# Kernel optimization log

Measured on AMD Instinct MI355X. Metric: run time of the kernel, lower is better.

Reference implementation:

```python
import jax, jax.numpy as jnp
import numpy as np

N, E, B = 50000, 400000, 64
N_INC, E_OUTC, U_INC, G_INC = 64, 64, 32, 64
H1A, H1B = 128, 64           # node_model_mlp1_hidden_sizes
H2 = 256                     # node_model_mlp2_hidden_sizes[0]
DIM_LH, DIM_L, N_OUTC = 128, 32, 64
LN_EPS = 1e-5

def _lin_init(key, din, dout):
    k1, k2 = jax.random.split(key)
    bound = 1.0 / np.sqrt(din)
    W = jax.random.uniform(k1, (din, dout), jnp.float32, -bound, bound)
    b = jax.random.uniform(k2, (dout,), jnp.float32, -bound, bound)
    return W, b

def setup_inputs() -> dict:
    key = jax.random.key(0)
    ks = jax.random.split(key, 16)
    x = jax.random.normal(ks[0], (N, N_INC), jnp.float32)
    edge_index = jax.random.randint(ks[1], (2, E), 0, N, jnp.int64)
    edge_attr = jax.random.normal(ks[2], (E, E_OUTC), jnp.float32)
    u = jax.random.normal(ks[3], (B, U_INC), jnp.float32)
    batch = jnp.sort(jax.random.randint(ks[4], (N,), 0, B, jnp.int64))
    goal = jax.random.normal(ks[5], (N, G_INC), jnp.float32)
    W1, b1 = _lin_init(ks[6], N_INC + E_OUTC, H1A)
    g1, be1 = jnp.ones((H1A,), jnp.float32), jnp.zeros((H1A,), jnp.float32)
    W2, b2 = _lin_init(ks[7], H1A, H1B)
    mlp2_inc = N_INC + H1B + U_INC
    W3, b3 = _lin_init(ks[8], mlp2_inc, H2)
    g3, be3 = jnp.ones((H2,), jnp.float32), jnp.zeros((H2,), jnp.float32)
    W4, b4 = _lin_init(ks[9], H2, DIM_LH)
    g4, be4 = jnp.ones((DIM_LH,), jnp.float32), jnp.zeros((DIM_LH,), jnp.float32)
    Wm, bm = _lin_init(ks[10], DIM_LH, DIM_L)
    Wv, bv = _lin_init(ks[11], DIM_LH, DIM_L)
    Wx, bx = _lin_init(ks[12], DIM_L, N_OUTC)
    return dict(x=x, edge_index=edge_index, edge_attr=edge_attr, u=u, batch=batch,
                goal=goal, W1=W1, b1=b1, g1=g1, be1=be1, W2=W2, b2=b2,
                W3=W3, b3=b3, g3=g3, be3=be3, W4=W4, b4=b4, g4=g4, be4=be4,
                Wm=Wm, bm=bm, Wv=Wv, bv=bv, Wx=Wx, bx=bx)

def _layernorm(h, g, b):
    mu = jnp.mean(h, axis=-1, keepdims=True)
    var = jnp.var(h, axis=-1, keepdims=True)
    return (h - mu) * jax.lax.rsqrt(var + LN_EPS) * g + b

def reference(x, edge_index, edge_attr, u, batch, goal,
              W1, b1, g1, be1, W2, b2,
              W3, b3, g3, be3, W4, b4, g4, be4,
              Wm, bm, Wv, bv, Wx, bx):
    row, col = edge_index[0], edge_index[1]
    # --- edge MLP: gather x[row], concat edge_attr, 2-layer MLP with LN+ReLU
    se = jnp.concatenate([x[row], edge_attr], axis=1)          # [E, n_inc+e_outc]
    h = jax.nn.relu(_layernorm(se @ W1 + b1, g1, be1)) @ W2 + b2  # [E, H1B]
    # --- scatter_mean over destination nodes
    sums = jax.ops.segment_sum(h, col, num_segments=N)          # [N, H1B]
    cnts = jax.ops.segment_sum(jnp.ones((E,), h.dtype), col, num_segments=N)
    aggs = sums / jnp.maximum(cnts, 1.0)[:, None]
    # --- node MLP 2
    z = jnp.concatenate([x, aggs, u[batch]], axis=1)            # [N, mlp2_inc]
    z = jax.nn.relu(_layernorm(z @ W3 + b3, g3, be3))
    z = jax.nn.relu(_layernorm(z @ W4 + b4, g4, be4))           # [N, DIM_LH]
    z_mu = z @ Wm + bm
    z_var = z @ Wv + bv                                         # log-variance
    eps = jax.random.normal(jax.random.key(42), z_mu.shape, z_mu.dtype)
    z_s = z_mu + eps * jnp.exp(0.5 * z_var)                     # reparameterize
    out = z_s @ Wx + bx                                         # [N, n_outc]
    return (out, z_mu, z_var)
```

## Files before the change

### kernel.cpp

```cpp
#include <hip/hip_runtime.h>

#define NN 50000
#define EE 400000
#define NB 49

typedef __attribute__((ext_vector_type(8))) short bf16x8;
typedef __attribute__((ext_vector_type(4))) float f32x4;

__device__ __forceinline__ void fma4(float4& a, float s, const float4& w){
  a.x = fmaf(s, w.x, a.x);
  a.y = fmaf(s, w.y, a.y);
  a.z = fmaf(s, w.z, a.z);
  a.w = fmaf(s, w.w, a.w);
}

__device__ __forceinline__ unsigned short f2bf(float f){
  unsigned u = __float_as_uint(f);
  unsigned r = (u + 0x7fffu + ((u >> 16) & 1u)) >> 16;
  return (unsigned short)r;
}

__device__ __forceinline__ bf16x8 cvt8(float4 lo, float4 hi){
  bf16x8 r;
  r[0]=(short)f2bf(lo.x); r[1]=(short)f2bf(lo.y); r[2]=(short)f2bf(lo.z); r[3]=(short)f2bf(lo.w);
  r[4]=(short)f2bf(hi.x); r[5]=(short)f2bf(hi.y); r[6]=(short)f2bf(hi.z); r[7]=(short)f2bf(hi.w);
  return r;
}

__device__ __forceinline__ unsigned packhl(float v){
  unsigned hi = f2bf(v);
  float fh = __uint_as_float(hi << 16);
  unsigned lo = f2bf(v - fh);
  return (hi << 16) | lo;
}

__device__ __forceinline__ uint4 pack4(float4 v){
  uint4 p;
  p.x = packhl(v.x); p.y = packhl(v.y); p.z = packhl(v.z); p.w = packhl(v.w);
  return p;
}

__device__ __forceinline__ void unpack8(uint4 p0, uint4 p1, bf16x8& hi, bf16x8& lo){
  hi[0]=(short)(p0.x>>16); lo[0]=(short)(p0.x & 0xffffu);
  hi[1]=(short)(p0.y>>16); lo[1]=(short)(p0.y & 0xffffu);
  hi[2]=(short)(p0.z>>16); lo[2]=(short)(p0.z & 0xffffu);
  hi[3]=(short)(p0.w>>16); lo[3]=(short)(p0.w & 0xffffu);
  hi[4]=(short)(p1.x>>16); lo[4]=(short)(p1.x & 0xffffu);
  hi[5]=(short)(p1.y>>16); lo[5]=(short)(p1.y & 0xffffu);
  hi[6]=(short)(p1.z>>16); lo[6]=(short)(p1.z & 0xffffu);
  hi[7]=(short)(p1.w>>16); lo[7]=(short)(p1.w & 0xffffu);
}

__device__ __forceinline__ unsigned rotl32(unsigned v, int d){ return (v<<d)|(v>>(32-d)); }

__device__ __forceinline__ float eps_at(unsigned idx){
  const unsigned k0 = 0u, k1 = 42u, k2 = 0x1BD11BDAu ^ 0u ^ 42u;
  unsigned x0 = 0u + k0, x1 = idx + k1;
  const int rotA[4] = {13,15,26,6};
  const int rotB[4] = {17,29,16,24};
  #pragma unroll
  for (int i=0;i<4;i++){ x0 += x1; x1 = rotl32(x1, rotA[i]); x1 ^= x0; }
  x0 += k1; x1 += k2 + 1u;
  #pragma unroll
  for (int i=0;i<4;i++){ x0 += x1; x1 = rotl32(x1, rotB[i]); x1 ^= x0; }
  x0 += k2; x1 += k0 + 2u;
  #pragma unroll
  for (int i=0;i<4;i++){ x0 += x1; x1 = rotl32(x1, rotA[i]); x1 ^= x0; }
  x0 += k0; x1 += k1 + 3u;
  #pragma unroll
  for (int i=0;i<4;i++){ x0 += x1; x1 = rotl32(x1, rotB[i]); x1 ^= x0; }
  x0 += k1; x1 += k2 + 4u;
  #pragma unroll
  for (int i=0;i<4;i++){ x0 += x1; x1 = rotl32(x1, rotA[i]); x1 ^= x0; }
  x0 += k2; x1 += k0 + 5u;
  unsigned bits = x0 ^ x1;
  float f = __uint_as_float((bits >> 9) | 0x3f800000u) - 1.0f;
  const float lo = -0.99999994f;
  float u = f * 2.0f + lo;
  u = fmaxf(u, lo);
  float w = -log1pf(-u*u);
  float p;
  if (w < 5.0f){
    w -= 2.5f;
    p = 2.81022636e-08f;
    p = fmaf(p,w, 3.43273939e-07f);
    p = fmaf(p,w,-3.5233877e-06f);
    p = fmaf(p,w,-4.39150654e-06f);
    p = fmaf(p,w, 0.00021858087f);
    p = fmaf(p,w,-0.00125372503f);
    p = fmaf(p,w,-0.00417768164f);
    p = fmaf(p,w, 0.246640727f);
    p = fmaf(p,w, 1.50140941f);
  } else {
    w = sqrtf(w) - 3.0f;
    p = -0.000200214257f;
    p = fmaf(p,w, 0.000100950558f);
    p = fmaf(p,w, 0.00134934322f);
    p = fmaf(p,w,-0.00367342844f);
    p = fmaf(p,w, 0.00573950773f);
    p = fmaf(p,w,-0.0076224613f);
    p = fmaf(p,w, 0.00943887047f);
    p = fmaf(p,w, 1.00167406f);
    p = fmaf(p,w, 2.83297682f);
  }
  return 1.41421356237f * (p * u);
}

__global__ __launch_bounds__(256) void k_prep_x(const float* __restrict__ x,
                                                unsigned short* __restrict__ xb){
  int t = blockIdx.x*256 + threadIdx.x;
  if (t < NN*64/8){
    const float4* p = (const float4*)(x + t*8);
    bf16x8 v = cvt8(p[0], p[1]);
    *(bf16x8*)(xb + t*8) = v;
  }
}

__global__ __launch_bounds__(256) void k_prep_w(const float* __restrict__ W1,
                                                const float* __restrict__ W2,
                                                unsigned short* __restrict__ W1T,
                                                unsigned short* __restrict__ W2T){
  for (int i = threadIdx.x; i < 128*128; i += 256){
    int n = i >> 7, k = i & 127;
    W1T[i] = f2bf(W1[k*128 + n]);
  }
  for (int i = threadIdx.x; i < 64*128; i += 256){
    int n = i >> 7, k = i & 127;
    W2T[i] = f2bf(W2[k*64 + n]);
  }
}

__global__ __launch_bounds__(256) void k_prep_w34(const float* __restrict__ W3,
                                                  const float* __restrict__ W4,
                                                  unsigned short* __restrict__ W3Th,
                                                  unsigned short* __restrict__ W3Tl,
                                                  unsigned short* __restrict__ W4Th,
                                                  unsigned short* __restrict__ W4Tl){
  int b = blockIdx.x;
  if (b < 256){
    int n = b;
    for (int k = threadIdx.x; k < 160; k += 256){
      float w = W3[k*256 + n];
      unsigned h = f2bf(w);
      float fh = __uint_as_float(h << 16);
      W3Th[n*160 + k] = (unsigned short)h;
      W3Tl[n*160 + k] = f2bf(w - fh);
    }
  } else {
    int n = b - 256;
    int k = threadIdx.x;
    float w = W4[k*128 + n];
    unsigned h = f2bf(w);
    float fh = __uint_as_float(h << 16);
    W4Th[n*256 + k] = (unsigned short)h;
    W4Tl[n*256 + k] = f2bf(w - fh);
  }
}

__global__ __launch_bounds__(256) void k_hist(const int* __restrict__ ei, int* __restrict__ cnt){
  int e = blockIdx.x*256 + threadIdx.x;
  if (e < EE) atomicAdd(&cnt[ei[EE + e]], 1);
}

__global__ __launch_bounds__(256) void k_scan1(const int* __restrict__ cnt,
                                               int* __restrict__ offs,
                                               int* __restrict__ partials){
  __shared__ int sdata[256];
  const int t = threadIdx.x, b = blockIdx.x;
  const int base = b*1024 + t*4;
  int v0 = (base+0 < NN) ? cnt[base+0] : 0;
  int v1 = (base+1 < NN) ? cnt[base+1] : 0;
  int v2 = (base+2 < NN) ? cnt[base+2] : 0;
  int v3 = (base+3 < NN) ? cnt[base+3] : 0;
  int tsum = v0+v1+v2+v3;
  sdata[t] = tsum;
  __syncthreads();
  for (int off=1; off<256; off<<=1){
    int add = (t >= off) ? sdata[t-off] : 0;
    __syncthreads();
    sdata[t] += add;
    __syncthreads();
  }
  int run = sdata[t] - tsum;
  if (base+0 < NN) offs[base+0] = run;  run += v0;
  if (base+1 < NN) offs[base+1] = run;  run += v1;
  if (base+2 < NN) offs[base+2] = run;  run += v2;
  if (base+3 < NN) offs[base+3] = run;
  if (t == 255) partials[b] = sdata[255];
}

__global__ __launch_bounds__(64) void k_scan2(int* __restrict__ partials){
  int l = threadIdx.x;
  int v = (l < NB) ? partials[l] : 0;
  int inc = v;
  #pragma unroll
  for (int off=1; off<64; off<<=1){
    int t = __shfl_up(inc, off);
    if (l >= off) inc += t;
  }
  if (l < NB) partials[l] = inc - v;
}

__global__ __launch_bounds__(256) void k_scan3(int* __restrict__ offs,
                                               const int* __restrict__ partials,
                                               int* __restrict__ cursor){
  const int t = threadIdx.x, b = blockIdx.x;
  const int base = b*1024 + t*4;
  int add = partials[b];
  #pragma unroll
  for (int k=0;k<4;k++){
    int i = base + k;
    if (i < NN){ int o = offs[i] + add; offs[i] = o; cursor[i] = o; }
  }
}

__global__ __launch_bounds__(256) void k_fill(const int* __restrict__ ei,
                                              int* __restrict__ cursor,
                                              int* __restrict__ epos){
  int e = blockIdx.x*256 + threadIdx.x;
  if (e < EE){
    int c = ei[EE + e];
    epos[e] = atomicAdd(&cursor[c], 1);
  }
}

#define H1STR 132
__global__ __launch_bounds__(256, 4) void k_edge(const int* __restrict__ ei,
    const float* __restrict__ ea,
    const unsigned short* __restrict__ xb,
    const unsigned short* __restrict__ W1T, const float* __restrict__ b1,
    const float* __restrict__ g1, const float* __restrict__ be1,
    const unsigned short* __restrict__ W2T, const float* __restrict__ b2,
    const int* __restrict__ epos,
    float* __restrict__ h_ws){
  __shared__ __align__(16) float h1[64*H1STR];
  __shared__ int rows_l[64];
  __shared__ int slot_l[64];
  const int tid  = threadIdx.x;
  const int base = blockIdx.x * 64;
  const int wv   = tid >> 6;
  const int lane = tid & 63;
  const int quad = lane >> 4;
  const int l16  = lane & 15;
  if (tid < 64) rows_l[tid] = ei[base + tid];
  if (tid >= 128 && tid < 192) slot_l[tid-128] = epos[base + tid - 128];
  __syncthreads();
  {
    int rw[4];
    #pragma unroll
    for (int m=0;m<4;m++) rw[m] = rows_l[m*16 + l16];
    f32x4 acc[4][2];
    #pragma unroll
    for (int m=0;m<4;m++){ acc[m][0] = (f32x4){0.f,0.f,0.f,0.f}; acc[m][1] = (f32x4){0.f,0.f,0.f,0.f}; }
    #pragma unroll
    for (int ks=0; ks<4; ks++){
      bf16x8 af[4];
      if (ks < 2){
        #pragma unroll
        for (int m=0;m<4;m++)
          af[m] = *(const bf16x8*)(xb + (size_t)rw[m]*64 + ks*32 + quad*8);
      } else {
        #pragma unroll
        for (int m=0;m<4;m++){
          const float* p = ea + (size_t)(base + m*16 + l16)*64 + (ks-2)*32 + quad*8;
          af[m] = cvt8(*(const float4*)p, *(const float4*)(p+4));
        }
      }
      bf16x8 bf0 = *(const bf16x8*)(W1T + (size_t)((2*wv+0)*16 + l16)*128 + ks*32 + quad*8);
      bf16x8 bf1 = *(const bf16x8*)(W1T + (size_t)((2*wv+1)*16 + l16)*128 + ks*32 + quad*8);
      #pragma unroll
      for (int m=0;m<4;m++){
        acc[m][0] = __builtin_amdgcn_mfma_f32_16x16x32_bf16(af[m], bf0, acc[m][0], 0, 0, 0);
        acc[m][1] = __builtin_amdgcn_mfma_f32_16x16x32_bf16(af[m], bf1, acc[m][1], 0, 0, 0);
      }
    }
    #pragma unroll
    for (int nl=0; nl<2; nl++){
      float b1c = b1[(2*wv+nl)*16 + l16];
      #pragma unroll
      for (int m=0;m<4;m++){
        #pragma unroll
        for (int r=0;r<4;r++)
          h1[(m*16 + quad*4 + r)*H1STR + (2*wv+nl)*16 + l16] = acc[m][nl][r] + b1c;
      }
    }
  }
  __syncthreads();
  {
    const float gA = g1[lane], gB = g1[lane+64];
    const float bA = be1[lane], bB = be1[lane+64];
    for (int r = wv*16; r < wv*16 + 16; ++r){
      float a = h1[r*H1STR + lane];
      float b = h1[r*H1STR + 64 + lane];
      float s = a + b, ss = fmaf(a,a,b*b);
      #pragma unroll
      for (int off=32; off; off>>=1){
        s  += __shfl_xor(s, off);
        ss += __shfl_xor(ss, off);
      }
      float mean = s * (1.0f/128.0f);
      float var  = ss * (1.0f/128.0f) - mean*mean;
      float inv = rsqrtf(var + 1e-5f);
      h1[r*H1STR + lane]      = fmaxf(fmaf((a-mean)*inv, gA, bA), 0.f);
      h1[r*H1STR + 64 + lane] = fmaxf(fmaf((b-mean)*inv, gB, bB), 0.f);
    }
  }
  __syncthreads();
  {
    f32x4 acc2[4];
    #pragma unroll
    for (int m=0;m<4;m++) acc2[m] = (f32x4){0.f,0.f,0.f,0.f};
    #pragma unroll
    for (int ks=0; ks<4; ks++){
      bf16x8 bfr = *(const bf16x8*)(W2T + (size_t)(wv*16 + l16)*128 + ks*32 + quad*8);
      #pragma unroll
      for (int m=0;m<4;m++){
        const float* p = h1 + (m*16 + l16)*H1STR + ks*32 + quad*8;
        bf16x8 af = cvt8(*(const float4*)p, *(const float4*)(p+4));
        acc2[m] = __builtin_amdgcn_mfma_f32_16x16x32_bf16(af, bfr, acc2[m], 0, 0, 0);
      }
    }
    float b2c = b2[wv*16 + l16];
    #pragma unroll
    for (int m=0;m<4;m++){
      #pragma unroll
      for (int r=0;r<4;r++)
        h_ws[(size_t)slot_l[m*16 + quad*4 + r]*64 + wv*16 + l16] = acc2[m][r] + b2c;
    }
  }
}

#define T2STR 132
#define ZSSTR 36
#define ZPSTR 164
#define H3STR 260
__global__ __launch_bounds__(256, 3) void k_node(const float* __restrict__ x,
    const float* __restrict__ u, const int* __restrict__ batch,
    const float* __restrict__ h_ws, const int* __restrict__ cnt,
    const int* __restrict__ offs,
    const unsigned short* __restrict__ W3Th, const unsigned short* __restrict__ W3Tl,
    const float* __restrict__ b3,
    const float* __restrict__ g3, const float* __restrict__ be3,
    const unsigned short* __restrict__ W4Th, const unsigned short* __restrict__ W4Tl,
    const float* __restrict__ b4,
    const float* __restrict__ g4, const float* __restrict__ be4,
    const float* __restrict__ Wm, const float* __restrict__ bm,
    const float* __restrict__ Wv, const float* __restrict__ bv,
    const float* __restrict__ Wx, const float* __restrict__ bx,
    float* __restrict__ out){
  __shared__ __align__(16) char arena[(32*H3STR + 32*ZPSTR)*4];
  float*    h3f = (float*)arena;
  unsigned* h3p = (unsigned*)arena;
  unsigned* zPK = (unsigned*)(arena + 32*H3STR*4);
  float*    t2S = (float*)(arena + 32*H3STR*4);

  const int tid = threadIdx.x;
  const int base = blockIdx.x * 32;
  const int wv   = tid >> 6;
  const int lane = tid & 63;
  const int quad = lane >> 4;
  const int l16  = lane & 15;

  #pragma unroll
  for (int i=0;i<2;i++){
    int l = tid + 256*i;
    int r = l >> 4, c4 = (l & 15) * 4;
    int n = base + r;
    float4 v = make_float4(0.f,0.f,0.f,0.f);
    if (n < NN) v = *(const float4*)(x + (size_t)n*64 + c4);
    *(uint4*)(zPK + r*ZPSTR + c4) = pack4(v);
  }
  {
    int r = tid >> 3, c4 = (tid & 7) * 4;
    int n = base + r;
    float4 v = make_float4(0.f,0.f,0.f,0.f);
    if (n < NN) v = *(const float4*)(u + (size_t)batch[n]*32 + c4);
    *(uint4*)(zPK + r*ZPSTR + 128 + c4) = pack4(v);
  }
  {
    int r = tid >> 3, p = tid & 7;
    int n = base + r;
    float4 a0 = make_float4(0.f,0.f,0.f,0.f), a1 = a0;
    int deg = 0;
    if (n < NN){
      deg = cnt[n];
      const float* hp = h_ws + (size_t)offs[n]*64 + p*8;
      int j = 0;
      for (; j + 2 <= deg; j += 2){
        float4 v0 = *(const float4*)(hp);
        float4 v1 = *(const float4*)(hp + 4);
        float4 w0 = *(const float4*)(hp + 64);
        float4 w1 = *(const float4*)(hp + 68);
        hp += 128;
        a0.x += v0.x; a0.y += v0.y; a0.z += v0.z; a0.w += v0.w;
        a1.x += v1.x; a1.y += v1.y; a1.z += v1.z; a1.w += v1.w;
        a0.x += w0.x; a0.y += w0.y; a0.z += w0.z; a0.w += w0.w;
        a1.x += w1.x; a1.y += w1.y; a1.z += w1.z; a1.w += w1.w;
      }
      if (j < deg){
        float4 v0 = *(const float4*)(hp);
        float4 v1 = *(const float4*)(hp + 4);
        a0.x += v0.x; a0.y += v0.y; a0.z += v0.z; a0.w += v0.w;
        a1.x += v1.x; a1.y += v1.y; a1.z += v1.z; a1.w += v1.w;
      }
    }
    float rc = 1.0f / fmaxf((float)deg, 1.0f);
    a0.x*=rc; a0.y*=rc; a0.z*=rc; a0.w*=rc;
    a1.x*=rc; a1.y*=rc; a1.z*=rc; a1.w*=rc;
    *(uint4*)(zPK + r*ZPSTR + 64 + p*8)     = pack4(a0);
    *(uint4*)(zPK + r*ZPSTR + 64 + p*8 + 4) = pack4(a1);
  }
  __syncthreads();
  {
    const int mt = wv & 1;
    const int ng = wv >> 1;
    f32x4 acc[8];
    #pragma unroll
    for (int i=0;i<8;i++) acc[i] = (f32x4){0.f,0.f,0.f,0.f};
    #pragma unroll
    for (int ks=0; ks<5; ks++){
      const unsigned* ap = zPK + (mt*16 + l16)*ZPSTR + ks*32 + quad*8;
      uint4 p0 = *(const uint4*)ap;
      uint4 p1 = *(const uint4*)(ap + 4);
      bf16x8 ah, al;
      unpack8(p0, p1, ah, al);
      #pragma unroll
      for (int i=0;i<8;i++){
        int nt = ng*8 + i;
        bf16x8 bh = *(const bf16x8*)(W3Th + (size_t)(nt*16 + l16)*160 + ks*32 + quad*8);
        bf16x8 bl = *(const bf16x8*)(W3Tl + (size_t)(nt*16 + l16)*160 + ks*32 + quad*8);
        acc[i] = __builtin_amdgcn_mfma_f32_16x16x32_bf16(ah, bh, acc[i], 0, 0, 0);
        acc[i] = __builtin_amdgcn_mfma_f32_16x16x32_bf16(al, bh, acc[i], 0, 0, 0);
        acc[i] = __builtin_amdgcn_mfma_f32_16x16x32_bf16(ah, bl, acc[i], 0, 0, 0);
      }
    }
    #pragma unroll
    for (int i=0;i<8;i++){
      int nt = ng*8 + i;
      float bc = b3[nt*16 + l16];
      #pragma unroll
      for (int r=0;r<4;r++)
        h3f[(mt*16 + quad*4 + r)*H3STR + nt*16 + l16] = acc[i][r] + bc;
    }
  }
  __syncthreads();
  {
    float4 gg  = *(const float4*)(g3 + lane*4);
    float4 bet = *(const float4*)(be3 + lane*4);
    #pragma unroll
    for (int r=0;r<8;r++){
      int row = wv*8 + r;
      float4 v = *(const float4*)(h3f + row*H3STR + lane*4);
      float s  = v.x + v.y + v.z + v.w;
      float ss = fmaf(v.x,v.x, fmaf(v.y,v.y, fmaf(v.z,v.z, v.w*v.w)));
      #pragma unroll
      for (int off=32; off; off>>=1){ s += __shfl_xor(s,off); ss += __shfl_xor(ss,off); }
      float mean = s * (1.0f/256.0f);
      float inv  = rsqrtf(ss*(1.0f/256.0f) - mean*mean + 1e-5f);
      float4 o;
      o.x = fmaxf(fmaf((v.x-mean)*inv, gg.x, bet.x), 0.f);
      o.y = fmaxf(fmaf((v.y-mean)*inv, gg.y, bet.y), 0.f);
      o.z = fmaxf(fmaf((v.z-mean)*inv, gg.z, bet.z), 0.f);
      o.w = fmaxf(fmaf((v.w-mean)*inv, gg.w, bet.w), 0.f);
      *(uint4*)(h3p + row*H3STR + lane*4) = pack4(o);
    }
  }
  __syncthreads();
  {
    const int mt = wv & 1;
    const int np = wv >> 1;
    f32x4 acc[4];
    #pragma unroll
    for (int i=0;i<4;i++) acc[i] = (f32x4){0.f,0.f,0.f,0.f};
    #pragma unroll
    for (int ks=0; ks<8; ks++){
      const unsigned* ap = h3p + (mt*16 + l16)*H3STR + ks*32 + quad*8;
      uint4 p0 = *(const uint4*)ap;
      uint4 p1 = *(const uint4*)(ap + 4);
      bf16x8 ah, al;
      unpack8(p0, p1, ah, al);
      #pragma unroll
      for (int i=0;i<4;i++){
        int nt = np*4 + i;
        bf16x8 bh = *(const bf16x8*)(W4Th + (size_t)(nt*16 + l16)*256 + ks*32 + quad*8);
        bf16x8 bl = *(const bf16x8*)(W4Tl + (size_t)(nt*16 + l16)*256 + ks*32 + quad*8);
        acc[i] = __builtin_amdgcn_mfma_f32_16x16x32_bf16(ah, bh, acc[i], 0, 0, 0);
        acc[i] = __builtin_amdgcn_mfma_f32_16x16x32_bf16(al, bh, acc[i], 0, 0, 0);
        acc[i] = __builtin_amdgcn_mfma_f32_16x16x32_bf16(ah, bl, acc[i], 0, 0, 0);
      }
    }
    #pragma unroll
    for (int i=0;i<4;i++){
      int nt = np*4 + i;
      float bc = b4[nt*16 + l16];
      #pragma unroll
      for (int r=0;r<4;r++)
        t2S[(mt*16 + quad*4 + r)*T2STR + nt*16 + l16] = acc[i][r] + bc;
    }
  }
  __syncthreads();
  {
    const int jq = tid & 31, rb = tid >> 5;
    float4 gg  = *(const float4*)(g4 + 4*jq);
    float4 bet = *(const float4*)(be4 + 4*jq);
    #pragma unroll
    for (int r=0;r<4;r++){
      int row = rb*4 + r;
      float4 v = *(const float4*)(t2S + row*T2STR + 4*jq);
      float s  = v.x + v.y + v.z + v.w;
      float ss = fmaf(v.x,v.x, fmaf(v.y,v.y, fmaf(v.z,v.z, v.w*v.w)));
      #pragma unroll
      for (int off=16; off; off>>=1){ s += __shfl_xor(s,off); ss += __shfl_xor(ss,off); }
      float mean = s * (1.0f/128.0f);
      float inv  = rsqrtf(ss*(1.0f/128.0f) - mean*mean + 1e-5f);
      float4 o;
      o.x = fmaxf(fmaf((v.x-mean)*inv, gg.x, bet.x), 0.f);
      o.y = fmaxf(fmaf((v.y-mean)*inv, gg.y, bet.y), 0.f);
      o.z = fmaxf(fmaf((v.z-mean)*inv, gg.z, bet.z), 0.f);
      o.w = fmaxf(fmaf((v.w-mean)*inv, gg.w, bet.w), 0.f);
      *(float4*)(t2S + row*T2STR + 4*jq) = o;
    }
  }
  __syncthreads();
  {
    const int jq = tid & 15, rb = tid >> 4;
    const float* Wp = (jq < 8) ? Wm : Wv;
    const int cq = (jq & 7) * 4;
    float4 acc[2];
    #pragma unroll
    for (int r=0;r<2;r++) acc[r] = make_float4(0.f,0.f,0.f,0.f);
    for (int k=0;k<128;k+=4){
      float4 w0 = *(const float4*)(Wp + (k+0)*32 + cq);
      float4 w1 = *(const float4*)(Wp + (k+1)*32 + cq);
      float4 w2 = *(const float4*)(Wp + (k+2)*32 + cq);
      float4 w3 = *(const float4*)(Wp + (k+3)*32 + cq);
      #pragma unroll
      for (int r=0;r<2;r++){
        float4 z = *(const float4*)(t2S + (rb*2+r)*T2STR + k);
        fma4(acc[r], z.x, w0); fma4(acc[r], z.y, w1);
        fma4(acc[r], z.z, w2); fma4(acc[r], z.w, w3);
      }
    }
    const float* bp = (jq < 8) ? bm : bv;
    float4 bb = *(const float4*)(bp + cq);
    const long long sec = (jq < 8) ? (long long)NN*64 : ((long long)NN*64 + (long long)NN*32);
    #pragma unroll
    for (int r=0;r<2;r++){
      float4 v = acc[r];
      v.x += bb.x; v.y += bb.y; v.z += bb.z; v.w += bb.w;
      int rr = rb*2 + r;
      *(float4*)(h3f + rr*64 + ((jq<8)?0:32) + cq) = v;
      int n = base + rr;
      if (n < NN) *(float4*)(out + sec + (long long)n*32 + cq) = v;
    }
  }
  __syncthreads();
  #pragma unroll
  for (int i=0;i<4;i++){
    int l = tid + 256*i;
    int r = l >> 5, jj = l & 31;
    float mu = h3f[r*64 + jj];
    float lv = h3f[r*64 + 32 + jj];
    unsigned idx = (unsigned)((base + r)*32 + jj);
    float e = eps_at(idx);
    t2S[r*ZSSTR + jj] = fmaf(e, expf(0.5f*lv), mu);
  }
  __syncthreads();
  {
    const int jq = tid & 15, rb = tid >> 4;
    float4 acc[2];
    #pragma unroll
    for (int r=0;r<2;r++) acc[r] = make_float4(0.f,0.f,0.f,0.f);
    for (int k=0;k<32;k+=4){
      float4 w0 = *(const float4*)(Wx + (k+0)*64 + 4*jq);
      float4 w1 = *(const float4*)(Wx + (k+1)*64 + 4*jq);
      float4 w2 = *(const float4*)(Wx + (k+2)*64 + 4*jq);
      float4 w3 = *(const float4*)(Wx + (k+3)*64 + 4*jq);
      #pragma unroll
      for (int r=0;r<2;r++){
        float4 z = *(const float4*)(t2S + (rb*2+r)*ZSSTR + k);
        fma4(acc[r], z.x, w0); fma4(acc[r], z.y, w1);
        fma4(acc[r], z.z, w2); fma4(acc[r], z.w, w3);
      }
    }
    float4 bb = *(const float4*)(bx + 4*jq);
    #pragma unroll
    for (int r=0;r<2;r++){
      int n = base + rb*2 + r;
      if (n < NN){
        float4 v = acc[r];
        v.x += bb.x; v.y += bb.y; v.z += bb.z; v.w += bb.w;
        *(float4*)(out + (long long)n*64 + 4*jq) = v;
      }
    }
  }
}

extern "C" void kernel_launch(void* const* d_in, const int* in_sizes, int n_in,
                              void* d_out, int out_size, void* d_ws, size_t ws_size,
                              hipStream_t stream) {
  const float* x     = (const float*)d_in[0];
  const int*   ei    = (const int*)d_in[1];
  const float* ea    = (const float*)d_in[2];
  const float* u     = (const float*)d_in[3];
  const int*   batch = (const int*)d_in[4];
  const float* W1 = (const float*)d_in[6];
  const float* b1 = (const float*)d_in[7];
  const float* g1 = (const float*)d_in[8];
  const float* be1= (const float*)d_in[9];
  const float* W2 = (const float*)d_in[10];
  const float* b2 = (const float*)d_in[11];
  const float* W3 = (const float*)d_in[12];
  const float* b3 = (const float*)d_in[13];
  const float* g3 = (const float*)d_in[14];
  const float* be3= (const float*)d_in[15];
  const float* W4 = (const float*)d_in[16];
  const float* b4 = (const float*)d_in[17];
  const float* g4 = (const float*)d_in[18];
  const float* be4= (const float*)d_in[19];
  const float* Wm = (const float*)d_in[20];
  const float* bm = (const float*)d_in[21];
  const float* Wv = (const float*)d_in[22];
  const float* bv = (const float*)d_in[23];
  const float* Wx = (const float*)d_in[24];
  const float* bx = (const float*)d_in[25];

  char* W = (char*)d_ws;
  size_t off = 0;
  float* h_ws = (float*)(W + off);  off += (size_t)EE*64*4;
  int* cnt      = (int*)(W + off);  off += (size_t)NN*4;
  int* offs     = (int*)(W + off);  off += (size_t)NN*4;
  int* cursor   = (int*)(W + off);  off += (size_t)NN*4;
  int* epos     = (int*)(W + off);  off += (size_t)EE*4;
  int* partials = (int*)(W + off);  off += 256;
  unsigned short* xb  = (unsigned short*)(W + off); off += (size_t)NN*64*2;
  unsigned short* W1T = (unsigned short*)(W + off); off += 128*128*2;
  unsigned short* W2T = (unsigned short*)(W + off); off += 64*128*2;
  unsigned short* W3Th = (unsigned short*)(W + off); off += 256*160*2;
  unsigned short* W3Tl = (unsigned short*)(W + off); off += 256*160*2;
  unsigned short* W4Th = (unsigned short*)(W + off); off += 128*256*2;
  unsigned short* W4Tl = (unsigned short*)(W + off); off += 128*256*2;
  float* out = (float*)d_out;

  hipMemsetAsync(cnt, 0, (size_t)NN*sizeof(int), stream);

  k_prep_x<<<(NN*64/8 + 255)/256, 256, 0, stream>>>(x, xb);
  k_prep_w<<<1, 256, 0, stream>>>(W1, W2, W1T, W2T);
  k_prep_w34<<<384, 256, 0, stream>>>(W3, W4, W3Th, W3Tl, W4Th, W4Tl);
  k_hist <<<(EE+255)/256, 256, 0, stream>>>(ei, cnt);
  k_scan1<<<NB, 256, 0, stream>>>(cnt, offs, partials);
  k_scan2<<<1, 64, 0, stream>>>(partials);
  k_scan3<<<NB, 256, 0, stream>>>(offs, partials, cursor);
  k_fill <<<(EE+255)/256, 256, 0, stream>>>(ei, cursor, epos);

  k_edge<<<EE/64, 256, 0, stream>>>(ei, ea, xb, W1T, b1, g1, be1, W2T, b2, epos, h_ws);
  k_node<<<(NN+31)/32, 256, 0, stream>>>(x, u, batch, h_ws, cnt, offs,
                                         W3Th, W3Tl, b3, g3, be3,
                                         W4Th, W4Tl, b4, g4, be4,
                                         Wm,bm, Wv,bv, Wx,bx, out);
}
```

Before: 572.3 us.

## Store edge messages as bf16 and split aggregation into separate high-occupancy kernel

The edge kernel now writes its per-edge MLP output as bf16 instead of fp32, which halves the 400k×64 workspace write and the later gather read. The aggregation, x/u packing and scatter-mean move out of the node kernel into a new k_agg kernel launched with high occupancy. That kernel writes a packed hi/lo z buffer that k_node reads straight from global memory, freeing LDS in k_node. The cost is an extra launch, a round trip of the z buffer through global memory, and lower precision on the edge messages before they are summed. Tail rows of the last node block read unwritten padding in zg, but those rows are presumably masked out on output.

```diff
diff --git a/kernel.cpp b/kernel.cpp
--- a/kernel.cpp
+++ b/kernel.cpp
@@ -50,6 +50,9 @@
   hi[6]=(short)(p1.z>>16); lo[6]=(short)(p1.z & 0xffffu);
   hi[7]=(short)(p1.w>>16); lo[7]=(short)(p1.w & 0xffffu);
 }
+
+__device__ __forceinline__ float blo(unsigned u){ return __uint_as_float(u << 16); }
+__device__ __forceinline__ float bhi(unsigned u){ return __uint_as_float(u & 0xffff0000u); }
 
 __device__ __forceinline__ unsigned rotl32(unsigned v, int d){ return (v<<d)|(v>>(32-d)); }
 
@@ -232,7 +235,7 @@
     const float* __restrict__ g1, const float* __restrict__ be1,
     const unsigned short* __restrict__ W2T, const float* __restrict__ b2,
     const int* __restrict__ epos,
-    float* __restrict__ h_ws){
+    unsigned short* __restrict__ h_ws){
   __shared__ __align__(16) float h1[64*H1STR];
   __shared__ int rows_l[64];
   __shared__ int slot_l[64];
@@ -325,19 +328,62 @@
     for (int m=0;m<4;m++){
       #pragma unroll
       for (int r=0;r<4;r++)
-        h_ws[(size_t)slot_l[m*16 + quad*4 + r]*64 + wv*16 + l16] = acc2[m][r] + b2c;
-    }
-  }
+        h_ws[(size_t)slot_l[m*16 + quad*4 + r]*64 + wv*16 + l16] = f2bf(acc2[m][r] + b2c);
+    }
+  }
+}
+
+__global__ __launch_bounds__(256, 8) void k_agg(const float* __restrict__ x,
+    const float* __restrict__ u, const int* __restrict__ batch,
+    const unsigned short* __restrict__ h_ws, const int* __restrict__ cnt,
+    const int* __restrict__ offs, unsigned* __restrict__ zg){
+  int t = blockIdx.x*256 + threadIdx.x;
+  int n = t >> 3, p = t & 7;
+  if (n >= NN) return;
+  unsigned* zr = zg + (size_t)n*160;
+  {
+    const float4* xp = (const float4*)(x + (size_t)n*64 + p*8);
+    *(uint4*)(zr + p*8)     = pack4(xp[0]);
+    *(uint4*)(zr + p*8 + 4) = pack4(xp[1]);
+  }
+  {
+    const float4* up = (const float4*)(u + (size_t)batch[n]*32 + p*4);
+    *(uint4*)(zr + 128 + p*4) = pack4(up[0]);
+  }
+  float a0=0.f,a1=0.f,a2=0.f,a3=0.f,a4=0.f,a5=0.f,a6=0.f,a7=0.f;
+  int deg = cnt[n];
+  const unsigned short* hp = h_ws + (size_t)offs[n]*64 + p*8;
+  int j = 0;
+  for (; j + 4 <= deg; j += 4){
+    uint4 v0 = *(const uint4*)(hp);
+    uint4 v1 = *(const uint4*)(hp + 64);
+    uint4 v2 = *(const uint4*)(hp + 128);
+    uint4 v3 = *(const uint4*)(hp + 192);
+    hp += 256;
+    a0 += blo(v0.x); a1 += bhi(v0.x); a2 += blo(v0.y); a3 += bhi(v0.y);
+    a4 += blo(v0.z); a5 += bhi(v0.z); a6 += blo(v0.w); a7 += bhi(v0.w);
+    a0 += blo(v1.x); a1 += bhi(v1.x); a2 += blo(v1.y); a3 += bhi(v1.y);
+    a4 += blo(v1.z); a5 += bhi(v1.z); a6 += blo(v1.w); a7 += bhi(v1.w);
+    a0 += blo(v2.x); a1 += bhi(v2.x); a2 += blo(v2.y); a3 += bhi(v2.y);
+    a4 += blo(v2.z); a5 += bhi(v2.z); a6 += blo(v2.w); a7 += bhi(v2.w);
+    a0 += blo(v3.x); a1 += bhi(v3.x); a2 += blo(v3.y); a3 += bhi(v3.y);
+    a4 += blo(v3.z); a5 += bhi(v3.z); a6 += blo(v3.w); a7 += bhi(v3.w);
+  }
+  for (; j < deg; ++j){
+    uint4 v = *(const uint4*)(hp);
+    hp += 64;
+    a0 += blo(v.x); a1 += bhi(v.x); a2 += blo(v.y); a3 += bhi(v.y);
+    a4 += blo(v.z); a5 += bhi(v.z); a6 += blo(v.w); a7 += bhi(v.w);
+  }
+  float rc = 1.0f / fmaxf((float)deg, 1.0f);
+  *(uint4*)(zr + 64 + p*8)     = pack4(make_float4(a0*rc, a1*rc, a2*rc, a3*rc));
+  *(uint4*)(zr + 64 + p*8 + 4) = pack4(make_float4(a4*rc, a5*rc, a6*rc, a7*rc));
 }
 
 #define T2STR 132
 #define ZSSTR 36
-#define ZPSTR 164
 #define H3STR 260
-__global__ __launch_bounds__(256, 3) void k_node(const float* __restrict__ x,
-    const float* __restrict__ u, const int* __restrict__ batch,
-    const float* __restrict__ h_ws, const int* __restrict__ cnt,
-    const int* __restrict__ offs,
+__global__ __launch_bounds__(256, 3) void k_node(const unsigned* __restrict__ zg,
     const unsigned short* __restrict__ W3Th, const unsigned short* __restrict__ W3Tl,
     const float* __restrict__ b3,
     const float* __restrict__ g3, const float* __restrict__ be3,
@@ -348,10 +394,9 @@
     const float* __restrict__ Wv, const float* __restrict__ bv,
     const float* __restrict__ Wx, const float* __restrict__ bx,
     float* __restrict__ out){
-  __shared__ __align__(16) char arena[(32*H3STR + 32*ZPSTR)*4];
+  __shared__ __align__(16) char arena[(32*H3STR + 32*T2STR)*4];
   float*    h3f = (float*)arena;
   unsigned* h3p = (unsigned*)arena;
-  unsigned* zPK = (unsigned*)(arena + 32*H3STR*4);
   float*    t2S = (float*)(arena + 32*H3STR*4);
 
   const int tid = threadIdx.x;
@@ -361,67 +406,17 @@
   const int quad = lane >> 4;
   const int l16  = lane & 15;
 
-  #pragma unroll
-  for (int i=0;i<2;i++){
-    int l = tid + 256*i;
-    int r = l >> 4, c4 = (l & 15) * 4;
-    int n = base + r;
-    float4 v = make_float4(0.f,0.f,0.f,0.f);
-    if (n < NN) v = *(const float4*)(x + (size_t)n*64 + c4);
-    *(uint4*)(zPK + r*ZPSTR + c4) = pack4(v);
-  }
-  {
-    int r = tid >> 3, c4 = (tid & 7) * 4;
-    int n = base + r;
-    float4 v = make_float4(0.f,0.f,0.f,0.f);
-    if (n < NN) v = *(const float4*)(u + (size_t)batch[n]*32 + c4);
-    *(uint4*)(zPK + r*ZPSTR + 128 + c4) = pack4(v);
-  }
-  {
-    int r = tid >> 3, p = tid & 7;
-    int n = base + r;
-    float4 a0 = make_float4(0.f,0.f,0.f,0.f), a1 = a0;
-    int deg = 0;
-    if (n < NN){
-      deg = cnt[n];
-      const float* hp = h_ws + (size_t)offs[n]*64 + p*8;
-      int j = 0;
-      for (; j + 2 <= deg; j += 2){
-        float4 v0 = *(const float4*)(hp);
-        float4 v1 = *(const float4*)(hp + 4);
-        float4 w0 = *(const float4*)(hp + 64);
-        float4 w1 = *(const float4*)(hp + 68);
-        hp += 128;
-        a0.x += v0.x; a0.y += v0.y; a0.z += v0.z; a0.w += v0.w;
-        a1.x += v1.x; a1.y += v1.y; a1.z += v1.z; a1.w += v1.w;
-        a0.x += w0.x; a0.y += w0.y; a0.z += w0.z; a0.w += w0.w;
-        a1.x += w1.x; a1.y += w1.y; a1.z += w1.z; a1.w += w1.w;
-      }
-      if (j < deg){
-        float4 v0 = *(const float4*)(hp);
-        float4 v1 = *(const float4*)(hp + 4);
-        a0.x += v0.x; a0.y += v0.y; a0.z += v0.z; a0.w += v0.w;
-        a1.x += v1.x; a1.y += v1.y; a1.z += v1.z; a1.w += v1.w;
-      }
-    }
-    float rc = 1.0f / fmaxf((float)deg, 1.0f);
-    a0.x*=rc; a0.y*=rc; a0.z*=rc; a0.w*=rc;
-    a1.x*=rc; a1.y*=rc; a1.z*=rc; a1.w*=rc;
-    *(uint4*)(zPK + r*ZPSTR + 64 + p*8)     = pack4(a0);
-    *(uint4*)(zPK + r*ZPSTR + 64 + p*8 + 4) = pack4(a1);
-  }
-  __syncthreads();
   {
     const int mt = wv & 1;
     const int ng = wv >> 1;
+    const unsigned* az = zg + (size_t)(base + mt*16 + l16)*160 + quad*8;
     f32x4 acc[8];
     #pragma unroll
     for (int i=0;i<8;i++) acc[i] = (f32x4){0.f,0.f,0.f,0.f};
     #pragma unroll
     for (int ks=0; ks<5; ks++){
-      const unsigned* ap = zPK + (mt*16 + l16)*ZPSTR + ks*32 + quad*8;
-      uint4 p0 = *(const uint4*)ap;
-      uint4 p1 = *(const uint4*)(ap + 4);
+      uint4 p0 = *(const uint4*)(az + ks*32);
+      uint4 p1 = *(const uint4*)(az + ks*32 + 4);
       bf16x8 ah, al;
       unpack8(p0, p1, ah, al);
       #pragma unroll
@@ -627,7 +622,7 @@
 
   char* W = (char*)d_ws;
   size_t off = 0;
-  float* h_ws = (float*)(W + off);  off += (size_t)EE*64*4;
+  unsigned short* h_ws = (unsigned short*)(W + off); off += (size_t)EE*64*2;
   int* cnt      = (int*)(W + off);  off += (size_t)NN*4;
   int* offs     = (int*)(W + off);  off += (size_t)NN*4;
   int* cursor   = (int*)(W + off);  off += (size_t)NN*4;
@@ -640,6 +635,8 @@
   unsigned short* W3Tl = (unsigned short*)(W + off); off += 256*160*2;
   unsigned short* W4Th = (unsigned short*)(W + off); off += 128*256*2;
   unsigned short* W4Tl = (unsigned short*)(W + off); off += 128*256*2;
+  off = (off + 255) & ~(size_t)255;
+  unsigned* zg = (unsigned*)(W + off); off += (size_t)(NN + 32)*160*4;
   float* out = (float*)d_out;
 
   hipMemsetAsync(cnt, 0, (size_t)NN*sizeof(int), stream);
@@ -654,7 +651,8 @@
   k_fill <<<(EE+255)/256, 256, 0, stream>>>(ei, cursor, epos);
 
   k_edge<<<EE/64, 256, 0, stream>>>(ei, ea, xb, W1T, b1, g1, be1, W2T, b2, epos, h_ws);
-  k_node<<<(NN+31)/32, 256, 0, stream>>>(x, u, batch, h_ws, cnt, offs,
+  k_agg <<<(NN*8 + 255)/256, 256, 0, stream>>>(x, u, batch, h_ws, cnt, offs, zg);
+  k_node<<<(NN+31)/32, 256, 0, stream>>>(zg,
                                          W3Th, W3Tl, b3, g3, be3,
                                          W4Th, W4Tl, b4, g4, be4,
                                          Wm,bm, Wv,bv, Wx,bx, out);
```

After: 560.8 us. 2.0% less time.
